# Kernel tuning notes

Measured on AMD Instinct MI355X. Metric: run time of the kernel, lower is better.

## Reference

```python
import jax, jax.numpy as jnp
import numpy as np

NUM_HEADS = 16

def setup_inputs() -> dict:
    key = jax.random.key(0)
    ks = jax.random.split(key, 6)
    d_in, d_out = 1024, 1024
    x = jax.random.normal(ks[0], (4, 2048, d_in), dtype=jnp.float32)
    s = 0.02
    Wq = jax.random.normal(ks[1], (d_in, d_out), dtype=jnp.float32) * s
    Wk = jax.random.normal(ks[2], (d_in, d_out), dtype=jnp.float32) * s
    Wv = jax.random.normal(ks[3], (d_in, d_out), dtype=jnp.float32) * s
    Wo = jax.random.normal(ks[4], (d_out, d_out), dtype=jnp.float32) * s
    bo = jnp.zeros((d_out,), dtype=jnp.float32)
    return {"x": x, "Wq": Wq, "Wk": Wk, "Wv": Wv, "Wo": Wo, "bo": bo}

def reference(x, Wq, Wk, Wv, Wo, bo):
    b, n, _ = x.shape
    h = NUM_HEADS
    hd = Wq.shape[1] // h
    # project and split heads: [b, h, n, hd]
    def split(t):
        return t.reshape(b, n, h, hd).transpose(0, 2, 1, 3)
    q = split(x @ Wq)
    k = split(x @ Wk)
    v = split(x @ Wv)
    scores = jnp.einsum('bhqd,bhkd->bhqk', q, k)
    causal = jnp.tril(jnp.ones((n, n), dtype=bool))  # True = keep
    scores = jnp.where(causal, scores, -jnp.inf)
    att = jax.nn.softmax(scores / jnp.sqrt(jnp.float32(hd)), axis=-1)
    out = jnp.einsum('bhqk,bhkd->bhqd', att, v)
    out = out.transpose(0, 2, 1, 3).reshape(b, n, h * hd)
    return out @ Wo + bo
```

## Files before the change

### kernel.cpp

```cpp
#include <hip/hip_runtime.h>
#include <math.h>

namespace {
constexpr int NB = 4;
constexpr int NS = 2048;
constexpr int DM = 1024;
constexpr int NH = 16;
constexpr int DH = 64;
constexpr int M  = NB * NS;

typedef __bf16 bf16x8 __attribute__((ext_vector_type(8)));
typedef float  floatx4 __attribute__((ext_vector_type(4)));

__device__ __forceinline__ ushort f2bf(float f) {
    uint u = __float_as_uint(f);
    return (ushort)((u + 0x7FFFu + ((u >> 16) & 1u)) >> 16);
}
__device__ __forceinline__ uint cvt_pk_bf16(float lo, float hi) {
    uint r;
    asm("v_cvt_pk_bf16_f32 %0, %1, %2" : "=v"(r) : "v"(lo), "v"(hi));
    return r;
}
__device__ __forceinline__ float fast_exp2(float x) {
#if __has_builtin(__builtin_amdgcn_exp2f)
    return __builtin_amdgcn_exp2f(x);
#else
    return exp2f(x);
#endif
}
__device__ __forceinline__ void gload16(const void* g, void* l) {
    __builtin_amdgcn_global_load_lds(
        (const __attribute__((address_space(1))) unsigned int*)g,
        (__attribute__((address_space(3))) unsigned int*)l, 16, 0, 0);
}

__global__ __launch_bounds__(256) void conv_x_k(const float* __restrict__ in,
                                                ushort* __restrict__ out) {
    int i = blockIdx.x * 256 + threadIdx.x;
    float4 v = ((const float4*)in)[i];
    ushort4 o;
    o.x = f2bf(v.x); o.y = f2bf(v.y); o.z = f2bf(v.z); o.w = f2bf(v.w);
    ((ushort4*)out)[i] = o;
}

__global__ __launch_bounds__(256) void conv_wt4_k(const float* __restrict__ W0,
                                                  const float* __restrict__ W1,
                                                  const float* __restrict__ W2,
                                                  const float* __restrict__ W3,
                                                  ushort* __restrict__ T0,
                                                  ushort* __restrict__ T1,
                                                  ushort* __restrict__ T2,
                                                  ushort* __restrict__ T3) {
    __shared__ float tile[64][65];
    const int z = blockIdx.z;
    const float* W = (z == 0) ? W0 : (z == 1) ? W1 : (z == 2) ? W2 : W3;
    ushort* Wt     = (z == 0) ? T0 : (z == 1) ? T1 : (z == 2) ? T2 : T3;
    const int t = threadIdx.x;
    const int k0 = blockIdx.y * 64, n0 = blockIdx.x * 64;
    #pragma unroll
    for (int i = 0; i < 16; ++i) {
        int idx = i * 256 + t, r = idx >> 6, c = idx & 63;
        tile[r][c] = W[(size_t)(k0 + r) * DM + n0 + c];
    }
    __syncthreads();
    #pragma unroll
    for (int i = 0; i < 16; ++i) {
        int idx = i * 256 + t, r = idx >> 6, c = idx & 63;
        Wt[(size_t)(n0 + r) * DM + k0 + c] = f2bf(tile[c][r]);
    }
}

template<int MODE>
__global__ __launch_bounds__(256) void mm_bf16_k(const ushort* __restrict__ A,
                                                 const ushort* __restrict__ Bt,
                                                 const float* __restrict__ bias,
                                                 void* __restrict__ outp,
                                                 float oscale) {
    __shared__ __align__(16) ushort As[2 * 128 * 32];
    __shared__ __align__(16) ushort Bs[2 * 128 * 32];
    const int t  = threadIdx.x;
    const int l  = t & 63;
    const int w  = t >> 6;
    const int wr = w >> 1, wc = w & 1;
    const int lr = l & 15, lg = l >> 4;

    const int nwg = gridDim.x * gridDim.y;
    const int lin = blockIdx.y * gridDim.x + blockIdx.x;
    const int id2 = (lin & 7) * (nwg >> 3) + (lin >> 3);
    const int row0 = (id2 / gridDim.x) * 128;
    const int col0 = (id2 % gridDim.x) * 128;

    floatx4 acc[4][4];
    #pragma unroll
    for (int m = 0; m < 4; ++m)
        #pragma unroll
        for (int n = 0; n < 4; ++n) acc[m][n] = (floatx4){0.f, 0.f, 0.f, 0.f};

    #pragma unroll
    for (int i = 0; i < 2; ++i) {
        int c = i * 256 + t, r = c >> 2, cb = (c & 3) * 16;
        gload16((const char*)A  + (size_t)(row0 + r) * 2048 + cb,
                (char*)As + c * 16);
        gload16((const char*)Bt + (size_t)(col0 + r) * 2048 + cb,
                (char*)Bs + c * 16);
    }
    int cur = 0;

    for (int k0 = 0; k0 < DM; k0 += 32) {
        __syncthreads();
        if (k0 + 32 < DM) {
            const int nb = cur ^ 1;
            #pragma unroll
            for (int i = 0; i < 2; ++i) {
                int c = i * 256 + t, r = c >> 2, cb = (c & 3) * 16;
                gload16((const char*)A  + (size_t)(row0 + r) * 2048 + (size_t)(k0 + 32) * 2 + cb,
                        (char*)As + nb * 8192 + c * 16);
                gload16((const char*)Bt + (size_t)(col0 + r) * 2048 + (size_t)(k0 + 32) * 2 + cb,
                        (char*)Bs + nb * 8192 + c * 16);
            }
        }

        const ushort* abase = As + cur * 4096 + (wr * 64 + lr) * 32 + lg * 8;
        const ushort* bbase = Bs + cur * 4096 + (wc * 64 + lr) * 32 + lg * 8;
        bf16x8 af[4], bfv[4];
        #pragma unroll
        for (int m = 0; m < 4; ++m)
            af[m] = *(const bf16x8*)(abase + m * 16 * 32);
        #pragma unroll
        for (int n = 0; n < 4; ++n)
            bfv[n] = *(const bf16x8*)(bbase + n * 16 * 32);
        #pragma unroll
        for (int m = 0; m < 4; ++m)
            #pragma unroll
            for (int n = 0; n < 4; ++n)
                acc[m][n] = __builtin_amdgcn_mfma_f32_16x16x32_bf16(
                    af[m], bfv[n], acc[m][n], 0, 0, 0);
        cur ^= 1;
    }

    #pragma unroll
    for (int m = 0; m < 4; ++m) {
        #pragma unroll
        for (int n = 0; n < 4; ++n) {
            floatx4 d = acc[m][n];
            #pragma unroll
            for (int r = 0; r < 4; ++r) {
                int grow = row0 + wr * 64 + m * 16 + lg * 4 + r;
                int gcol = col0 + wc * 64 + n * 16 + lr;
                if (MODE == 1) {
                    ((float*)outp)[(size_t)grow * DM + gcol] = d[r] + bias[gcol];
                } else if (MODE == 2) {
                    int h = grow >> 6,  dd = grow & 63;
                    int b = gcol >> 11, nn = gcol & (NS - 1);
                    int k6 = nn & 63;
                    int np = (nn & ~63) | (k6 & 3) | (((k6 >> 5) & 1) << 2) |
                             (((k6 >> 2) & 3) << 3) | (((k6 >> 4) & 1) << 5);
                    ((ushort*)outp)[((size_t)(b * NH + h) * DH + dd) * NS + np] = f2bf(d[r]);
                } else {
                    int which = gcol >> 10;
                    int col = gcol & 1023;
                    int b = grow >> 11, nn = grow & (NS - 1);
                    int h = col >> 6,  dd = col & 63;
                    float sc = which ? 1.f : oscale;
                    ((ushort*)outp)[(size_t)which * M * DM +
                        (((size_t)(b * NH + h)) * NS + nn) * DH + dd] = f2bf(d[r] * sc);
                }
            }
        }
    }
}

__global__ __launch_bounds__(256, 4) void attn_k(const ushort* __restrict__ Q,
                                                 const ushort* __restrict__ K,
                                                 const ushort* __restrict__ Vt,
                                                 ushort* __restrict__ O) {
    __shared__ __align__(16) ushort K_lds[2 * 64 * 64];
    __shared__ __align__(16) ushort V_lds[2 * 64 * 64];

    const int t    = threadIdx.x;
    const int w    = t >> 6;
    const int l    = t & 63;
    const int lr   = l & 15;
    const int lg   = l >> 4;
    const int bh   = blockIdx.x;
    const int yp = blockIdx.y & 3, yr = blockIdx.y >> 2;
    const int qblk = (yr == 0) ? 15 - yp
                   : (yr == 1) ? 8 + yp
                   : (yr == 2) ? 4 + (yp ^ 1)
                               : (yp ^ 2);
    const size_t base = (size_t)bh * NS * DH;
    const int b = bh >> 4, h = bh & 15;

    const int srow_lo = l >> 3;
    const int gs      = (l & 7) ^ srow_lo;

    const int qbase  = qblk * 128;
    const int qmin_w = qbase + w * 32;
    const int qmax_w = qmin_w + 31;
    const int ntiles = 2 * (qblk + 1);

    bf16x8 qb[2][2];
    #pragma unroll
    for (int nq = 0; nq < 2; ++nq)
        #pragma unroll
        for (int kk2 = 0; kk2 < 2; ++kk2)
            qb[nq][kk2] = *(const bf16x8*)&Q[base +
                (size_t)(qbase + w * 32 + nq * 16 + lr) * DH + kk2 * 32 + lg * 8];

    uint4 ones_u = make_uint4(0x3F803F80u, 0x3F803F80u, 0x3F803F80u, 0x3F803F80u);
    bf16x8 ones_b = *(const bf16x8*)&ones_u;

    floatx4 acc[2][4];
    #pragma unroll
    for (int nq = 0; nq < 2; ++nq)
        #pragma unroll
        for (int nd = 0; nd < 4; ++nd) acc[nq][nd] = (floatx4){0.f, 0.f, 0.f, 0.f};
    floatx4 accl[2];
    accl[0] = (floatx4){0.f, 0.f, 0.f, 0.f};
    accl[1] = (floatx4){0.f, 0.f, 0.f, 0.f};
    const floatx4 z4 = (floatx4){0.f, 0.f, 0.f, 0.f};

    const char* kg0 = (const char*)(K + base + (size_t)(w * 8 + srow_lo) * DH) + gs * 16;
    const char* kg1 = kg0 + (size_t)32 * DH * 2;
    const char* vg0 = (const char*)(Vt + base + (size_t)(w * 8 + srow_lo) * NS) + gs * 16;
    const char* vg1 = vg0 + (size_t)32 * NS * 2;
    char* kl0 = (char*)K_lds + w * 1024 + l * 16;
    char* kl1 = kl0 + 4096;
    char* vl0 = (char*)V_lds + w * 1024 + l * 16;
    char* vl1 = vl0 + 4096;

    gload16(kg0, kl0); gload16(vg0, vl0);
    gload16(kg1, kl1); gload16(vg1, vl1);
    kg0 += 8192; kg1 += 8192; vg0 += 128; vg1 += 128;
    int cur = 0;

    for (int tile = 0; tile < ntiles; ++tile) {
        const int kv0 = tile * 64;
        __syncthreads();
        if (tile + 1 < ntiles) {
            const int nb = cur ^ 1;
            gload16(kg0, kl0 + nb * 8192); gload16(vg0, vl0 + nb * 8192);
            gload16(kg1, kl1 + nb * 8192); gload16(vg1, vl1 + nb * 8192);
            kg0 += 8192; kg1 += 8192; vg0 += 128; vg1 += 128;
        }

        if (kv0 <= qmax_w) {
            floatx4 s[4][2];
            __builtin_amdgcn_s_setprio(1);
            {
                bf16x8 ka[4];
                #pragma unroll
                for (int m = 0; m < 4; ++m)
                    ka[m] = *(const bf16x8*)((const char*)K_lds + cur * 8192 +
                        (m * 16 + lr) * 128 + ((lg ^ (lr & 7)) * 16));
                #pragma unroll
                for (int m = 0; m < 4; ++m)
                    #pragma unroll
                    for (int nq = 0; nq < 2; ++nq)
                        s[m][nq] = __builtin_amdgcn_mfma_f32_16x16x32_bf16(
                            ka[m], qb[nq][0], z4, 0, 0, 0);
                #pragma unroll
                for (int m = 0; m < 4; ++m)
                    ka[m] = *(const bf16x8*)((const char*)K_lds + cur * 8192 +
                        (m * 16 + lr) * 128 + (((4 + lg) ^ (lr & 7)) * 16));
                #pragma unroll
                for (int m = 0; m < 4; ++m)
                    #pragma unroll
                    for (int nq = 0; nq < 2; ++nq)
                        s[m][nq] = __builtin_amdgcn_mfma_f32_16x16x32_bf16(
                            ka[m], qb[nq][1], s[m][nq], 0, 0, 0);
            }
            __builtin_amdgcn_s_setprio(0);

            const bool need_mask = (kv0 + 63 > qmin_w);
            const int kb0 = kv0 + lg * 4;
            #pragma unroll
            for (int nq = 0; nq < 2; ++nq) {
                const int qn = qmin_w + nq * 16 + lr;
                #pragma unroll
                for (int m = 0; m < 4; ++m) {
                    #pragma unroll
                    for (int r = 0; r < 4; ++r) {
                        float v = s[m][nq][r];
                        if (need_mask)
                            v = ((kb0 + m * 16 + r) > qn) ? -INFINITY : v;
                        s[m][nq][r] = fast_exp2(v);
                    }
                }
            }

            __builtin_amdgcn_s_setprio(1);
            #pragma unroll
            for (int kk2 = 0; kk2 < 2; ++kk2) {
                const int m0 = kk2, m1 = kk2 + 2;
                bf16x8 vb[4];
                #pragma unroll
                for (int nd = 0; nd < 4; ++nd)
                    vb[nd] = *(const bf16x8*)((const char*)V_lds + cur * 8192 +
                        (nd * 16 + lr) * 128 + (((kk2 * 4 + lg) ^ (lr & 7)) * 16));
                #pragma unroll
                for (int nq = 0; nq < 2; ++nq) {
                    uint4 pk;
                    pk.x = cvt_pk_bf16(s[m0][nq][0], s[m0][nq][1]);
                    pk.y = cvt_pk_bf16(s[m0][nq][2], s[m0][nq][3]);
                    pk.z = cvt_pk_bf16(s[m1][nq][0], s[m1][nq][1]);
                    pk.w = cvt_pk_bf16(s[m1][nq][2], s[m1][nq][3]);
                    bf16x8 pa = *(const bf16x8*)&pk;
                    #pragma unroll
                    for (int nd = 0; nd < 4; ++nd)
                        acc[nq][nd] = __builtin_amdgcn_mfma_f32_16x16x32_bf16(
                            pa, vb[nd], acc[nq][nd], 0, 0, 0);
                    accl[nq] = __builtin_amdgcn_mfma_f32_16x16x32_bf16(
                        pa, ones_b, accl[nq], 0, 0, 0);
                }
            }
            __builtin_amdgcn_s_setprio(0);
        }
        cur ^= 1;
    }

    #pragma unroll
    for (int nq = 0; nq < 2; ++nq) {
        #pragma unroll
        for (int r = 0; r < 4; ++r) {
            float inv = 1.f / accl[nq][r];
            int q = qbase + w * 32 + nq * 16 + lg * 4 + r;
            ushort* op = &O[((size_t)(b * NS + q)) * DM + h * DH + lr];
            op[0]  = f2bf(acc[nq][0][r] * inv);
            op[16] = f2bf(acc[nq][1][r] * inv);
            op[32] = f2bf(acc[nq][2][r] * inv);
            op[48] = f2bf(acc[nq][3][r] * inv);
        }
    }
}

}

extern "C" void kernel_launch(void* const* d_in, const int* in_sizes, int n_in,
                              void* d_out, int out_size, void* d_ws, size_t ws_size,
                              hipStream_t stream) {
    const float* x  = (const float*)d_in[0];
    const float* Wq = (const float*)d_in[1];
    const float* Wk = (const float*)d_in[2];
    const float* Wv = (const float*)d_in[3];
    const float* Wo = (const float*)d_in[4];
    const float* bo = (const float*)d_in[5];
    float* out = (float*)d_out;

    ushort* xb  = (ushort*)d_ws;
    ushort* WqT = xb  + (size_t)M * DM;
    ushort* WkT = WqT + (size_t)DM * DM;
    ushort* WvT = WkT + (size_t)DM * DM;
    ushort* WoT = WvT + (size_t)DM * DM;
    ushort* Qb  = WoT + (size_t)DM * DM;
    ushort* Kb  = Qb  + (size_t)M * DM;
    ushort* Vtg = Kb  + (size_t)M * DM;
    ushort* Ab  = Vtg + (size_t)M * DM;

    const float SCALE_Q = 0.125f * 1.4426950408889634f;

    conv_x_k<<<M * DM / 4 / 256, 256, 0, stream>>>(x, xb);
    conv_wt4_k<<<dim3(DM / 64, DM / 64, 4), 256, 0, stream>>>(
        Wq, Wk, Wv, Wo, WqT, WkT, WvT, WoT);

    mm_bf16_k<3><<<dim3(2048 / 128, M / 128), 256, 0, stream>>>(xb, WqT, nullptr, Qb, SCALE_Q);
    mm_bf16_k<2><<<dim3(M / 128, DM / 128), 256, 0, stream>>>(WvT, xb, nullptr, Vtg, 1.f);
    attn_k<<<dim3(NB * NH, 16), 256, 0, stream>>>(Qb, Kb, Vtg, Ab);
    mm_bf16_k<1><<<dim3(DM / 128, M / 128), 256, 0, stream>>>(Ab, WoT, bo, out, 1.f);
}
```

Baseline: 163.1 us.

## Use two 64-row waves per attention block and process KV tile in halves

The attention kernel now runs 2 waves of 128 threads instead of 4, each wave owning 64 query rows instead of 32. Each K/V fragment read from LDS is therefore reused across more query rows, and each wave issues more of the cooperative K/V global loads. The 64-key tile is split into two 32-key halves, computing scores, exp and PV for each half in turn, to bound score register use. The cost is more registers per wave (larger accumulators), fewer waves per block for latency hiding, and coarser causal skipping because more masked work falls inside each wave's 64-row range.

```diff
diff --git a/kernel.cpp b/kernel.cpp
--- a/kernel.cpp
+++ b/kernel.cpp
@@ -170,7 +170,7 @@
     }
 }
 
-__global__ __launch_bounds__(256, 4) void attn_k(const ushort* __restrict__ Q,
+__global__ __launch_bounds__(128, 2) void attn_k(const ushort* __restrict__ Q,
                                                  const ushort* __restrict__ K,
                                                  const ushort* __restrict__ Vt,
                                                  ushort* __restrict__ O) {
@@ -195,43 +195,43 @@
     const int gs      = (l & 7) ^ srow_lo;
 
     const int qbase  = qblk * 128;
-    const int qmin_w = qbase + w * 32;
-    const int qmax_w = qmin_w + 31;
+    const int qmin_w = qbase + w * 64;
+    const int qmax_w = qmin_w + 63;
     const int ntiles = 2 * (qblk + 1);
 
-    bf16x8 qb[2][2];
-    #pragma unroll
-    for (int nq = 0; nq < 2; ++nq)
-        #pragma unroll
-        for (int kk2 = 0; kk2 < 2; ++kk2)
-            qb[nq][kk2] = *(const bf16x8*)&Q[base +
-                (size_t)(qbase + w * 32 + nq * 16 + lr) * DH + kk2 * 32 + lg * 8];
+    bf16x8 qb[4][2];
+    #pragma unroll
+    for (int nq = 0; nq < 4; ++nq)
+        #pragma unroll
+        for (int d2 = 0; d2 < 2; ++d2)
+            qb[nq][d2] = *(const bf16x8*)&Q[base +
+                (size_t)(qmin_w + nq * 16 + lr) * DH + d2 * 32 + lg * 8];
 
     uint4 ones_u = make_uint4(0x3F803F80u, 0x3F803F80u, 0x3F803F80u, 0x3F803F80u);
     bf16x8 ones_b = *(const bf16x8*)&ones_u;
 
-    floatx4 acc[2][4];
-    #pragma unroll
-    for (int nq = 0; nq < 2; ++nq)
+    floatx4 acc[4][4];
+    #pragma unroll
+    for (int nq = 0; nq < 4; ++nq)
         #pragma unroll
         for (int nd = 0; nd < 4; ++nd) acc[nq][nd] = (floatx4){0.f, 0.f, 0.f, 0.f};
-    floatx4 accl[2];
-    accl[0] = (floatx4){0.f, 0.f, 0.f, 0.f};
-    accl[1] = (floatx4){0.f, 0.f, 0.f, 0.f};
+    floatx4 accl[4];
+    #pragma unroll
+    for (int nq = 0; nq < 4; ++nq) accl[nq] = (floatx4){0.f, 0.f, 0.f, 0.f};
     const floatx4 z4 = (floatx4){0.f, 0.f, 0.f, 0.f};
 
-    const char* kg0 = (const char*)(K + base + (size_t)(w * 8 + srow_lo) * DH) + gs * 16;
-    const char* kg1 = kg0 + (size_t)32 * DH * 2;
-    const char* vg0 = (const char*)(Vt + base + (size_t)(w * 8 + srow_lo) * NS) + gs * 16;
-    const char* vg1 = vg0 + (size_t)32 * NS * 2;
-    char* kl0 = (char*)K_lds + w * 1024 + l * 16;
-    char* kl1 = kl0 + 4096;
-    char* vl0 = (char*)V_lds + w * 1024 + l * 16;
-    char* vl1 = vl0 + 4096;
-
-    gload16(kg0, kl0); gload16(vg0, vl0);
-    gload16(kg1, kl1); gload16(vg1, vl1);
-    kg0 += 8192; kg1 += 8192; vg0 += 128; vg1 += 128;
+    const char* kg = (const char*)(K + base + (size_t)srow_lo * DH) + gs * 16;
+    const char* vg = (const char*)(Vt + base + (size_t)srow_lo * NS) + gs * 16;
+    char* kl = (char*)K_lds + l * 16;
+    char* vl = (char*)V_lds + l * 16;
+
+    #pragma unroll
+    for (int i = 0; i < 4; ++i) {
+        const int cc = w + i * 2;
+        gload16(kg + cc * 1024,  kl + cc * 1024);
+        gload16(vg + cc * 32768, vl + cc * 1024);
+    }
+    kg += 8192; vg += 128;
     int cur = 0;
 
     for (int tile = 0; tile < ntiles; ++tile) {
@@ -239,92 +239,96 @@
         __syncthreads();
         if (tile + 1 < ntiles) {
             const int nb = cur ^ 1;
-            gload16(kg0, kl0 + nb * 8192); gload16(vg0, vl0 + nb * 8192);
-            gload16(kg1, kl1 + nb * 8192); gload16(vg1, vl1 + nb * 8192);
-            kg0 += 8192; kg1 += 8192; vg0 += 128; vg1 += 128;
+            #pragma unroll
+            for (int i = 0; i < 4; ++i) {
+                const int cc = w + i * 2;
+                gload16(kg + cc * 1024,  kl + nb * 8192 + cc * 1024);
+                gload16(vg + cc * 32768, vl + nb * 8192 + cc * 1024);
+            }
+            kg += 8192; vg += 128;
         }
 
         if (kv0 <= qmax_w) {
-            floatx4 s[4][2];
-            __builtin_amdgcn_s_setprio(1);
-            {
-                bf16x8 ka[4];
-                #pragma unroll
-                for (int m = 0; m < 4; ++m)
-                    ka[m] = *(const bf16x8*)((const char*)K_lds + cur * 8192 +
-                        (m * 16 + lr) * 128 + ((lg ^ (lr & 7)) * 16));
-                #pragma unroll
-                for (int m = 0; m < 4; ++m)
-                    #pragma unroll
-                    for (int nq = 0; nq < 2; ++nq)
-                        s[m][nq] = __builtin_amdgcn_mfma_f32_16x16x32_bf16(
-                            ka[m], qb[nq][0], z4, 0, 0, 0);
-                #pragma unroll
-                for (int m = 0; m < 4; ++m)
-                    ka[m] = *(const bf16x8*)((const char*)K_lds + cur * 8192 +
-                        (m * 16 + lr) * 128 + (((4 + lg) ^ (lr & 7)) * 16));
-                #pragma unroll
-                for (int m = 0; m < 4; ++m)
-                    #pragma unroll
-                    for (int nq = 0; nq < 2; ++nq)
-                        s[m][nq] = __builtin_amdgcn_mfma_f32_16x16x32_bf16(
-                            ka[m], qb[nq][1], s[m][nq], 0, 0, 0);
-            }
-            __builtin_amdgcn_s_setprio(0);
-
             const bool need_mask = (kv0 + 63 > qmin_w);
             const int kb0 = kv0 + lg * 4;
             #pragma unroll
-            for (int nq = 0; nq < 2; ++nq) {
-                const int qn = qmin_w + nq * 16 + lr;
+            for (int p = 0; p < 2; ++p) {
+                floatx4 sp[2][4];
+                __builtin_amdgcn_s_setprio(1);
+                {
+                    bf16x8 ka[4];
+                    #pragma unroll
+                    for (int j = 0; j < 2; ++j)
+                        #pragma unroll
+                        for (int d2 = 0; d2 < 2; ++d2)
+                            ka[j * 2 + d2] = *(const bf16x8*)((const char*)K_lds +
+                                cur * 8192 + ((p + 2 * j) * 16 + lr) * 128 +
+                                (((d2 * 4 + lg) ^ (lr & 7)) * 16));
+                    #pragma unroll
+                    for (int j = 0; j < 2; ++j)
+                        #pragma unroll
+                        for (int nq = 0; nq < 4; ++nq)
+                            sp[j][nq] = __builtin_amdgcn_mfma_f32_16x16x32_bf16(
+                                ka[j * 2 + 0], qb[nq][0], z4, 0, 0, 0);
+                    #pragma unroll
+                    for (int j = 0; j < 2; ++j)
+                        #pragma unroll
+                        for (int nq = 0; nq < 4; ++nq)
+                            sp[j][nq] = __builtin_amdgcn_mfma_f32_16x16x32_bf16(
+                                ka[j * 2 + 1], qb[nq][1], sp[j][nq], 0, 0, 0);
+                }
+                __builtin_amdgcn_s_setprio(0);
+
                 #pragma unroll
-                for (int m = 0; m < 4; ++m) {
-                    #pragma unroll
-                    for (int r = 0; r < 4; ++r) {
-                        float v = s[m][nq][r];
-                        if (need_mask)
-                            v = ((kb0 + m * 16 + r) > qn) ? -INFINITY : v;
-                        s[m][nq][r] = fast_exp2(v);
+                for (int nq = 0; nq < 4; ++nq) {
+                    const int qn = qmin_w + nq * 16 + lr;
+                    #pragma unroll
+                    for (int j = 0; j < 2; ++j) {
+                        #pragma unroll
+                        for (int r = 0; r < 4; ++r) {
+                            float v = sp[j][nq][r];
+                            if (need_mask)
+                                v = ((kb0 + (p + 2 * j) * 16 + r) > qn) ? -INFINITY : v;
+                            sp[j][nq][r] = fast_exp2(v);
+                        }
                     }
                 }
+
+                __builtin_amdgcn_s_setprio(1);
+                {
+                    bf16x8 vb[4];
+                    #pragma unroll
+                    for (int nd = 0; nd < 4; ++nd)
+                        vb[nd] = *(const bf16x8*)((const char*)V_lds + cur * 8192 +
+                            (nd * 16 + lr) * 128 + (((p * 4 + lg) ^ (lr & 7)) * 16));
+                    #pragma unroll
+                    for (int nq = 0; nq < 4; ++nq) {
+                        uint4 pk;
+                        pk.x = cvt_pk_bf16(sp[0][nq][0], sp[0][nq][1]);
+                        pk.y = cvt_pk_bf16(sp[0][nq][2], sp[0][nq][3]);
+                        pk.z = cvt_pk_bf16(sp[1][nq][0], sp[1][nq][1]);
+                        pk.w = cvt_pk_bf16(sp[1][nq][2], sp[1][nq][3]);
+                        bf16x8 pa = *(const bf16x8*)&pk;
+                        #pragma unroll
+                        for (int nd = 0; nd < 4; ++nd)
+                            acc[nq][nd] = __builtin_amdgcn_mfma_f32_16x16x32_bf16(
+                                pa, vb[nd], acc[nq][nd], 0, 0, 0);
+                        accl[nq] = __builtin_amdgcn_mfma_f32_16x16x32_bf16(
+                            pa, ones_b, accl[nq], 0, 0, 0);
+                    }
+                }
+                __builtin_amdgcn_s_setprio(0);
             }
-
-            __builtin_amdgcn_s_setprio(1);
-            #pragma unroll
-            for (int kk2 = 0; kk2 < 2; ++kk2) {
-                const int m0 = kk2, m1 = kk2 + 2;
-                bf16x8 vb[4];
-                #pragma unroll
-                for (int nd = 0; nd < 4; ++nd)
-                    vb[nd] = *(const bf16x8*)((const char*)V_lds + cur * 8192 +
-                        (nd * 16 + lr) * 128 + (((kk2 * 4 + lg) ^ (lr & 7)) * 16));
-                #pragma unroll
-                for (int nq = 0; nq < 2; ++nq) {
-                    uint4 pk;
-                    pk.x = cvt_pk_bf16(s[m0][nq][0], s[m0][nq][1]);
-                    pk.y = cvt_pk_bf16(s[m0][nq][2], s[m0][nq][3]);
-                    pk.z = cvt_pk_bf16(s[m1][nq][0], s[m1][nq][1]);
-                    pk.w = cvt_pk_bf16(s[m1][nq][2], s[m1][nq][3]);
-                    bf16x8 pa = *(const bf16x8*)&pk;
-                    #pragma unroll
-                    for (int nd = 0; nd < 4; ++nd)
-                        acc[nq][nd] = __builtin_amdgcn_mfma_f32_16x16x32_bf16(
-                            pa, vb[nd], acc[nq][nd], 0, 0, 0);
-                    accl[nq] = __builtin_amdgcn_mfma_f32_16x16x32_bf16(
-                        pa, ones_b, accl[nq], 0, 0, 0);
-                }
-            }
-            __builtin_amdgcn_s_setprio(0);
         }
         cur ^= 1;
     }
 
     #pragma unroll
-    for (int nq = 0; nq < 2; ++nq) {
+    for (int nq = 0; nq < 4; ++nq) {
         #pragma unroll
         for (int r = 0; r < 4; ++r) {
             float inv = 1.f / accl[nq][r];
-            int q = qbase + w * 32 + nq * 16 + lg * 4 + r;
+            int q = qmin_w + nq * 16 + lg * 4 + r;
             ushort* op = &O[((size_t)(b * NS + q)) * DM + h * DH + lr];
             op[0]  = f2bf(acc[nq][0][r] * inv);
             op[16] = f2bf(acc[nq][1][r] * inv);
@@ -365,6 +369,6 @@
 
     mm_bf16_k<3><<<dim3(2048 / 128, M / 128), 256, 0, stream>>>(xb, WqT, nullptr, Qb, SCALE_Q);
     mm_bf16_k<2><<<dim3(M / 128, DM / 128), 256, 0, stream>>>(WvT, xb, nullptr, Vtg, 1.f);
-    attn_k<<<dim3(NB * NH, 16), 256, 0, stream>>>(Qb, Kb, Vtg, Ab);
+    attn_k<<<dim3(NB * NH, 16), 128, 0, stream>>>(Qb, Kb, Vtg, Ab);
     mm_bf16_k<1><<<dim3(DM / 128, M / 128), 256, 0, stream>>>(Ab, WoT, bo, out, 1.f);
 }
```

Result: slower. 185.8 us (+14.0%).

## Split long causal attention query blocks across two KV halves with merge

Applied to the files above, without the earlier changes.

Query blocks 8-15, which have the most KV tiles under the causal mask, are each split into two workgroups that cover separate halves of the KV range and write unnormalized fp32 partial accumulators and row sums to workspace. A new merge kernel adds the two partials, normalizes, and writes bf16 output. The goal is to balance load and shorten the tail of the attention grid. The cost is an extra launch plus fp32 workspace traffic. The split path is taken only if the workspace is large enough.

```diff
diff --git a/kernel.cpp b/kernel.cpp
--- a/kernel.cpp
+++ b/kernel.cpp
@@ -8,6 +8,7 @@
 constexpr int NH = 16;
 constexpr int DH = 64;
 constexpr int M  = NB * NS;
+constexpr int PSZ = 128 * 64 + 128;
 
 typedef __bf16 bf16x8 __attribute__((ext_vector_type(8)));
 typedef float  floatx4 __attribute__((ext_vector_type(4)));
@@ -170,10 +171,12 @@
     }
 }
 
+template<int SPLIT>
 __global__ __launch_bounds__(256, 4) void attn_k(const ushort* __restrict__ Q,
                                                  const ushort* __restrict__ K,
                                                  const ushort* __restrict__ Vt,
-                                                 ushort* __restrict__ O) {
+                                                 ushort* __restrict__ O,
+                                                 float* __restrict__ pws) {
     __shared__ __align__(16) ushort K_lds[2 * 64 * 64];
     __shared__ __align__(16) ushort V_lds[2 * 64 * 64];
 
@@ -183,11 +186,24 @@
     const int lr   = l & 15;
     const int lg   = l >> 4;
     const int bh   = blockIdx.x;
-    const int yp = blockIdx.y & 3, yr = blockIdx.y >> 2;
-    const int qblk = (yr == 0) ? 15 - yp
-                   : (yr == 1) ? 8 + yp
-                   : (yr == 2) ? 4 + (yp ^ 1)
-                               : (yp ^ 2);
+
+    int qblk, half;
+    if constexpr (SPLIT) {
+        static const signed char q_tab[24] = {7,6,5,4, 0,1,2,3, 15,15,14,14,
+                                              8,8,9,9, 11,11,10,10, 12,12,13,13};
+        static const signed char h_tab[24] = {-1,-1,-1,-1, -1,-1,-1,-1, 0,1,0,1,
+                                              0,1,0,1, 0,1,0,1, 0,1,0,1};
+        qblk = q_tab[blockIdx.y];
+        half = h_tab[blockIdx.y];
+    } else {
+        const int yp = blockIdx.y & 3, yr = blockIdx.y >> 2;
+        qblk = (yr == 0) ? 15 - yp
+             : (yr == 1) ? 8 + yp
+             : (yr == 2) ? 4 + (yp ^ 1)
+                         : (yp ^ 2);
+        half = -1;
+    }
+
     const size_t base = (size_t)bh * NS * DH;
     const int b = bh >> 4, h = bh & 15;
 
@@ -197,7 +213,8 @@
     const int qbase  = qblk * 128;
     const int qmin_w = qbase + w * 32;
     const int qmax_w = qmin_w + 31;
-    const int ntiles = 2 * (qblk + 1);
+    const int t0 = (half == 1) ? (qblk + 1) : 0;
+    const int t1 = (half == 0) ? (qblk + 1) : 2 * (qblk + 1);
 
     bf16x8 qb[2][2];
     #pragma unroll
@@ -220,9 +237,11 @@
     accl[1] = (floatx4){0.f, 0.f, 0.f, 0.f};
     const floatx4 z4 = (floatx4){0.f, 0.f, 0.f, 0.f};
 
-    const char* kg0 = (const char*)(K + base + (size_t)(w * 8 + srow_lo) * DH) + gs * 16;
+    const char* kg0 = (const char*)(K + base + (size_t)(w * 8 + srow_lo) * DH) +
+                      gs * 16 + (size_t)t0 * 8192;
     const char* kg1 = kg0 + (size_t)32 * DH * 2;
-    const char* vg0 = (const char*)(Vt + base + (size_t)(w * 8 + srow_lo) * NS) + gs * 16;
+    const char* vg0 = (const char*)(Vt + base + (size_t)(w * 8 + srow_lo) * NS) +
+                      gs * 16 + (size_t)t0 * 128;
     const char* vg1 = vg0 + (size_t)32 * NS * 2;
     char* kl0 = (char*)K_lds + w * 1024 + l * 16;
     char* kl1 = kl0 + 4096;
@@ -234,10 +253,10 @@
     kg0 += 8192; kg1 += 8192; vg0 += 128; vg1 += 128;
     int cur = 0;
 
-    for (int tile = 0; tile < ntiles; ++tile) {
+    for (int tile = t0; tile < t1; ++tile) {
         const int kv0 = tile * 64;
         __syncthreads();
-        if (tile + 1 < ntiles) {
+        if (tile + 1 < t1) {
             const int nb = cur ^ 1;
             gload16(kg0, kl0 + nb * 8192); gload16(vg0, vl0 + nb * 8192);
             gload16(kg1, kl1 + nb * 8192); gload16(vg1, vl1 + nb * 8192);
@@ -319,19 +338,58 @@
         cur ^= 1;
     }
 
-    #pragma unroll
-    for (int nq = 0; nq < 2; ++nq) {
-        #pragma unroll
-        for (int r = 0; r < 4; ++r) {
-            float inv = 1.f / accl[nq][r];
-            int q = qbase + w * 32 + nq * 16 + lg * 4 + r;
-            ushort* op = &O[((size_t)(b * NS + q)) * DM + h * DH + lr];
-            op[0]  = f2bf(acc[nq][0][r] * inv);
-            op[16] = f2bf(acc[nq][1][r] * inv);
-            op[32] = f2bf(acc[nq][2][r] * inv);
-            op[48] = f2bf(acc[nq][3][r] * inv);
-        }
-    }
+    if (!SPLIT || half < 0) {
+        #pragma unroll
+        for (int nq = 0; nq < 2; ++nq) {
+            #pragma unroll
+            for (int r = 0; r < 4; ++r) {
+                float inv = 1.f / accl[nq][r];
+                int q = qbase + w * 32 + nq * 16 + lg * 4 + r;
+                ushort* op = &O[((size_t)(b * NS + q)) * DM + h * DH + lr];
+                op[0]  = f2bf(acc[nq][0][r] * inv);
+                op[16] = f2bf(acc[nq][1][r] * inv);
+                op[32] = f2bf(acc[nq][2][r] * inv);
+                op[48] = f2bf(acc[nq][3][r] * inv);
+            }
+        }
+    } else {
+        float* P = pws + ((size_t)half * 512 + (size_t)bh * 8 + (qblk - 8)) * PSZ;
+        #pragma unroll
+        for (int nq = 0; nq < 2; ++nq) {
+            #pragma unroll
+            for (int r = 0; r < 4; ++r) {
+                int row = w * 32 + nq * 16 + lg * 4 + r;
+                #pragma unroll
+                for (int nd = 0; nd < 4; ++nd)
+                    P[row * 64 + nd * 16 + lr] = acc[nq][nd][r];
+                if (lr == 0) P[128 * 64 + row] = accl[nq][r];
+            }
+        }
+    }
+}
+
+__global__ __launch_bounds__(256) void merge_k(const float* __restrict__ pws,
+                                               ushort* __restrict__ O) {
+    const int bh = blockIdx.x, j = blockIdx.y;
+    const int b = bh >> 4, h = bh & 15;
+    const float* P0 = pws + ((size_t)bh * 8 + j) * PSZ;
+    const float* P1 = pws + ((size_t)512 + (size_t)bh * 8 + j) * PSZ;
+    const int t = threadIdx.x;
+    const int row = t >> 1, c0 = (t & 1) * 32;
+    float inv = 1.f / (P0[128 * 64 + row] + P1[128 * 64 + row]);
+    const int q = (8 + j) * 128 + row;
+    ushort* op = &O[((size_t)(b * NS + q)) * DM + h * DH + c0];
+    uint o[16];
+    #pragma unroll
+    for (int i = 0; i < 8; ++i) {
+        float4 a  = *(const float4*)&P0[row * 64 + c0 + i * 4];
+        float4 bb = *(const float4*)&P1[row * 64 + c0 + i * 4];
+        o[i * 2]     = cvt_pk_bf16((a.x + bb.x) * inv, (a.y + bb.y) * inv);
+        o[i * 2 + 1] = cvt_pk_bf16((a.z + bb.z) * inv, (a.w + bb.w) * inv);
+    }
+    #pragma unroll
+    for (int i = 0; i < 4; ++i)
+        ((uint4*)op)[i] = make_uint4(o[i * 4], o[i * 4 + 1], o[i * 4 + 2], o[i * 4 + 3]);
 }
 
 }
@@ -356,6 +414,10 @@
     ushort* Kb  = Qb  + (size_t)M * DM;
     ushort* Vtg = Kb  + (size_t)M * DM;
     ushort* Ab  = Vtg + (size_t)M * DM;
+    float*  pws = (float*)(Ab + (size_t)M * DM);
+
+    const size_t needed = (size_t)((char*)(pws + (size_t)1024 * PSZ) - (char*)d_ws);
+    const bool do_split = (ws_size >= needed);
 
     const float SCALE_Q = 0.125f * 1.4426950408889634f;
 
@@ -365,6 +427,11 @@
 
     mm_bf16_k<3><<<dim3(2048 / 128, M / 128), 256, 0, stream>>>(xb, WqT, nullptr, Qb, SCALE_Q);
     mm_bf16_k<2><<<dim3(M / 128, DM / 128), 256, 0, stream>>>(WvT, xb, nullptr, Vtg, 1.f);
-    attn_k<<<dim3(NB * NH, 16), 256, 0, stream>>>(Qb, Kb, Vtg, Ab);
+    if (do_split) {
+        attn_k<1><<<dim3(NB * NH, 24), 256, 0, stream>>>(Qb, Kb, Vtg, Ab, pws);
+        merge_k<<<dim3(NB * NH, 8), 256, 0, stream>>>(pws, Ab);
+    } else {
+        attn_k<0><<<dim3(NB * NH, 16), 256, 0, stream>>>(Qb, Kb, Vtg, Ab, pws);
+    }
     mm_bf16_k<1><<<dim3(DM / 128, M / 128), 256, 0, stream>>>(Ab, WoT, bo, out, 1.f);
 }
```

Result: slower. 178.7 us (+9.6%).
